# Kernel tuning notes

Hardware: AMD Instinct MI355X
Metric: run time of the kernel (lower is better)

The kernel has to match this reference:

```python
import jax, jax.numpy as jnp
import numpy as np

PATCH = 14
N_HEAD = 8
TOP_K = 2

def _ln(x, g, b, eps=1e-5):
    m = jnp.mean(x, -1, keepdims=True)
    v = jnp.var(x, -1, keepdims=True)
    return (x - m) * jax.lax.rsqrt(v + eps) * g + b

def _mha(x, wq, bq, wk, bk, wv, bv, wo, bo):
    B, S, D = x.shape
    hd = D // N_HEAD
    def split(t):
        return t.reshape(B, S, N_HEAD, hd).transpose(0, 2, 1, 3)
    q = split(x @ wq + bq)
    k = split(x @ wk + bk)
    v = split(x @ wv + bv)
    scores = jnp.einsum('bhqd,bhkd->bhqk', q, k) / jnp.sqrt(jnp.asarray(hd, x.dtype))
    attn = jax.nn.softmax(scores, -1)  # [B,H,S,S]
    out = jnp.einsum('bhqk,bhkd->bhqd', attn, v).transpose(0, 2, 1, 3).reshape(B, S, D)
    return out @ wo + bo, attn

def _moe(x, rw, rb, w1, b1, w2, b2):
    # dense-compute-all-experts-then-mask, matching SparseMoE.forward
    B, S, D = x.shape
    E = rw.shape[1]
    probs = jax.nn.softmax(x @ rw + rb, -1)           # [B,S,E]
    topv, topi = jax.lax.top_k(probs, TOP_K)          # [B,S,K]
    oh = jax.nn.one_hot(topi, E, dtype=x.dtype)       # [B,S,K,E]
    mask = jnp.sum(oh * topv[..., None], -2)          # [B,S,E] top-k gates, zeros elsewhere
    h = jax.nn.gelu(jnp.einsum('bsd,edh->besh', x, w1) + b1[None, :, None, :], approximate=False)
    outs = jnp.einsum('besh,ehd->besd', h, w2) + b2[None, :, None, :]
    out = jnp.einsum('besd,bse->bsd', outs, mask)     # masked sum over experts
    # load-balancing auxiliary loss
    frac = jnp.mean(jnp.sum(oh, -2).reshape(-1, E), 0)
    imp = jnp.mean(probs.reshape(-1, E), 0)
    loss = E * jnp.sum(frac * imp)
    return out, loss

def setup_inputs():
    key = jax.random.key(0)
    B, C, IMG = 32, 3, 224
    D, E, HID = 512, 8, 2048
    S = (IMG // PATCH) ** 2
    PD = C * PATCH * PATCH
    ks = iter(jax.random.split(key, 64))
    def w(shape, fan):
        return jax.random.normal(next(ks), shape, jnp.float32) / np.sqrt(fan).astype(np.float32)
    def moe_params():
        return dict(rw=w((D, E), D), rb=jnp.zeros(E), w1=w((E, D, HID), D), b1=jnp.zeros((E, HID)), w2=w((E, HID, D), HID), b2=jnp.zeros((E, D)))
    m1 = moe_params(); m2 = moe_params()
    return dict(
        x=jax.random.normal(next(ks), (B, C, IMG, IMG), jnp.float32),
        pe_w=w((PD, D), PD), pe_b=jnp.zeros(D),
        pos=w((1, S, D), D),
        ln1_g=jnp.ones(D), ln1_b=jnp.zeros(D),
        ln2_g=jnp.ones(D), ln2_b=jnp.zeros(D),
        ln3_g=jnp.ones(D), ln3_b=jnp.zeros(D),
        wq=w((D, D), D), bq=jnp.zeros(D), wk=w((D, D), D), bk=jnp.zeros(D),
        wv=w((D, D), D), bv=jnp.zeros(D), wo=w((D, D), D), bo=jnp.zeros(D),
        m1_rw=m1['rw'], m1_rb=m1['rb'], m1_w1=m1['w1'], m1_b1=m1['b1'], m1_w2=m1['w2'], m1_b2=m1['b2'],
        m2_rw=m2['rw'], m2_rb=m2['rb'], m2_w1=m2['w1'], m2_b1=m2['b1'], m2_w2=m2['w2'], m2_b2=m2['b2'],
        cls_w=w((D, D), D), cls_b=jnp.zeros(D))

def reference(x, pe_w, pe_b, pos, ln1_g, ln1_b, ln2_g, ln2_b, ln3_g, ln3_b, wq, bq, wk, bk, wv, bv, wo, bo, m1_rw, m1_rb, m1_w1, m1_b1, m1_w2, m1_b2, m2_rw, m2_rb, m2_w1, m2_b1, m2_w2, m2_b2, cls_w, cls_b):
    B, C, H, W = x.shape
    h = H // PATCH
    # einops 'b c (h p1) (w p2) -> b (h w) (p1 p2 c)'
    patches = x.reshape(B, C, h, PATCH, h, PATCH).transpose(0, 2, 4, 3, 5, 1).reshape(B, h * h, PATCH * PATCH * C)
    e = patches @ pe_w + pe_b + pos
    sa, attn = _mha(_ln(e, ln1_g, ln1_b), wq, bq, wk, bk, wv, bv, wo, bo)
    e = e + sa  # dropout is identity at eval
    o1, l1 = _moe(_ln(e, ln2_g, ln2_b), m1_rw, m1_rb, m1_w1, m1_b1, m1_w2, m1_b2)
    o2, l2 = _moe(_ln(o1, ln3_g, ln3_b), m2_rw, m2_rb, m2_w1, m2_b1, m2_w2, m2_b2)
    fv = jnp.mean(o2, 1)
    logits = fv @ cls_w + cls_b
    attn_w = jax.nn.softmax(jnp.mean(attn, 1), -1)  # mean over heads then re-softmax, as in source
    return logits, fv, l1 + l2, attn_w
```

## Files before the change

kernel.cpp:

```cpp
#include <hip/hip_runtime.h>
#include <hip/hip_bf16.h>

using bf16 = __hip_bfloat16;
typedef unsigned short u16;
typedef __attribute__((ext_vector_type(8))) short short8;
typedef __attribute__((ext_vector_type(4))) float f32x4;

#define DEVFN __device__ __forceinline__

DEVFN u16 f2bu(float v) { return __builtin_bit_cast(u16, __float2bfloat16(v)); }
DEVFN float us2f(u16 u) { union { unsigned int i; float f; } x; x.i = ((unsigned int)u) << 16; return x.f; }
DEVFN void unp8(uint4 u, float* f) {
  f[0]=us2f(u.x & 0xffffu); f[1]=us2f(u.x >> 16);
  f[2]=us2f(u.y & 0xffffu); f[3]=us2f(u.y >> 16);
  f[4]=us2f(u.z & 0xffffu); f[5]=us2f(u.z >> 16);
  f[6]=us2f(u.w & 0xffffu); f[7]=us2f(u.w >> 16);
}

DEVFN f32x4 mfma16(short8 a, short8 b, f32x4 c) {
  return __builtin_amdgcn_mfma_f32_16x16x32_bf16(a, b, c, 0, 0, 0);
}

DEVFN void gl16(const u16* g, u16* l) {
  __builtin_amdgcn_global_load_lds((const __attribute__((address_space(1))) void*)g,
                                   (__attribute__((address_space(3))) void*)l, 16, 0, 0);
}

static constexpr size_t OF_PATCH = 0;
static constexpr size_t OF_E     = 4816896;
static constexpr size_t OF_XN    = 9011200;
static constexpr size_t OF_Q     = 13205504;
static constexpr size_t OF_FV    = 38371328;
static constexpr size_t OF_GATES = 38387712;
static constexpr size_t OF_IMPS  = 38404096;
static constexpr size_t OF_CNT   = 38404104;
static constexpr size_t OF_BASE  = 38404112;
static constexpr size_t OF_CURS  = 38404120;
static constexpr size_t OF_LOSS  = 38404128;
static constexpr size_t OF_TOPI  = 38404136;
static constexpr size_t OF_RPOS  = 38420520;
static constexpr size_t OF_RLIST = 38436904;
static constexpr size_t OF_Q16   = 13205504;
static constexpr size_t OF_K16   = 15302656;
static constexpr size_t OF_VT    = 17399808;
static constexpr size_t OF_CTX16 = 19496960;
static constexpr size_t OF_PET   = 21594112;
static constexpr size_t OF_WQT   = 21757952;
static constexpr size_t OF_WKT   = 21889024;
static constexpr size_t OF_WVT   = 22020096;
static constexpr size_t OF_WOT   = 22151168;
static constexpr size_t OF_O1    = 29982720;
static constexpr size_t OF_O2    = 34177024;

__global__ __launch_bounds__(256) void k_patchify(const float* __restrict__ x, u16* __restrict__ XP) {
  int idx = blockIdx.x * 256 + threadIdx.x;
  if (idx >= 8192 * 640) return;
  int row = idx / 640, j = idx - row * 640;
  u16 v = 0;
  if (j < 588) {
    int b = row >> 8, s = row & 255;
    int hh = s >> 4, ww = s & 15;
    int c = j % 3, tt = j / 3;
    int p2 = tt % 14, p1 = tt / 14;
    int src = ((b * 3 + c) * 224 + hh * 14 + p1) * 224 + (ww * 14 + p2);
    v = f2bu(x[src]);
  }
  XP[idx] = v;
}

__global__ __launch_bounds__(256) void k_wcvtd(const float* __restrict__ W, u16* __restrict__ WT, int K, int KP)
{
  __shared__ float s[32][33];
  const int t = threadIdx.x;
  const int tx = t & 31, ty = t >> 5;
  const int k0 = blockIdx.x * 32, n0 = blockIdx.y * 32;
#pragma unroll
  for (int i = 0; i < 4; i++) {
    int kk = k0 + ty + i * 8;
    s[ty + i * 8][tx] = (kk < K) ? W[(size_t)kk * 512 + n0 + tx] : 0.f;
  }
  __syncthreads();
#pragma unroll
  for (int i = 0; i < 4; i++) WT[(size_t)(n0 + ty + i * 8) * KP + k0 + tx] = f2bu(s[tx][ty + i * 8]);
}

__global__ __launch_bounds__(256) void k_wcvt(const float* __restrict__ W, u16* __restrict__ Wt, int K, int N)
{
  __shared__ float s[32][33];
  const int t = threadIdx.x;
  const int tx = t & 31, ty = t >> 5;
  const int k0 = blockIdx.x * 32, n0 = blockIdx.y * 32;
  const size_t es = (size_t)K * N;
  const float* We = W + (size_t)blockIdx.z * es;
  u16* Wte = Wt + (size_t)blockIdx.z * es;
#pragma unroll
  for (int i = 0; i < 4; i++) s[ty + i * 8][tx] = We[(size_t)(k0 + ty + i * 8) * N + n0 + tx];
  __syncthreads();
#pragma unroll
  for (int i = 0; i < 4; i++) Wte[(size_t)(n0 + ty + i * 8) * K + k0 + tx] = f2bu(s[tx][ty + i * 8]);
}

DEVFN void mma_loop(f32x4 acc[4][4], const u16* const agp[4], const u16* const bgp[4],
                    u16* const alp[4], u16* const blp[4], u16* As, u16* Bs,
                    int K, int wm, int wn, int ml, int kq)
{
  for (int k0 = 0; k0 < K; k0 += 64) {
    __syncthreads();
#pragma unroll
    for (int q = 0; q < 4; q++) { gl16(agp[q] + k0, alp[q]); gl16(bgp[q] + k0, blp[q]); }
    __syncthreads();
#pragma unroll
    for (int ks = 0; ks < 2; ks++) {
      const int c = ks * 4 + kq;
      short8 af[4], bf[4];
#pragma unroll
      for (int i = 0; i < 4; i++) {
        const int row = wm + i * 16 + ml;
        af[i] = *(const short8*)&As[row * 64 + ((c ^ (row & 7)) << 3)];
      }
#pragma unroll
      for (int j = 0; j < 4; j++) {
        const int row = wn + j * 16 + ml;
        bf[j] = *(const short8*)&Bs[row * 64 + ((c ^ (row & 7)) << 3)];
      }
#pragma unroll
      for (int i = 0; i < 4; i++)
#pragma unroll
        for (int j = 0; j < 4; j++) acc[i][j] = mfma16(af[i], bf[j], acc[i][j]);
    }
  }
}

DEVFN void ep_xpose(float* ep, const f32x4* ai, int kq, int ml, int er, int ec, float* v)
{
#pragma unroll
  for (int j = 0; j < 4; j++)
#pragma unroll
    for (int r = 0; r < 4; r++)
      ep[(kq * 4 + r) * 68 + j * 16 + ml] = ai[j][r];
  __syncthreads();
#pragma unroll
  for (int u = 0; u < 4; u++) {
    float4 f = *(const float4*)&ep[er * 68 + ec + u * 4];
    v[u * 4 + 0] = f.x; v[u * 4 + 1] = f.y; v[u * 4 + 2] = f.z; v[u * 4 + 3] = f.w;
  }
  __syncthreads();
}

template<int MODE>
__global__ __launch_bounds__(256) void k_bgemm(const u16* __restrict__ A, const u16* __restrict__ BT,
    const float* __restrict__ bias, float* __restrict__ Cf, u16* __restrict__ O16,
    const float* __restrict__ pos, int K)
{
  const int m0 = blockIdx.y * 128, n0 = blockIdx.x * 128;
  __shared__ u16 SB[16384];
  u16* As = SB; u16* Bs = SB + 8192;
  const int t = threadIdx.x;
  const int widx = t >> 6, lane = t & 63;
  const int wm = (widx & 1) * 64, wn = (widx >> 1) * 64;
  const int ml = lane & 15, kq = lane >> 4;
  const u16* agp[4]; const u16* bgp[4]; u16* alp[4]; u16* blp[4];
#pragma unroll
  for (int q = 0; q < 4; q++) {
    const int slot = q * 256 + t;
    const int row = slot >> 3;
    const int c = (slot & 7) ^ (row & 7);
    agp[q] = A + (size_t)(m0 + row) * K + c * 8;
    bgp[q] = BT + (size_t)(n0 + row) * K + c * 8;
    alp[q] = &As[(q * 256 + widx * 64) * 8];
    blp[q] = &Bs[(q * 256 + widx * 64) * 8];
  }
  f32x4 acc[4][4];
#pragma unroll
  for (int i = 0; i < 4; i++)
#pragma unroll
    for (int j = 0; j < 4; j++) acc[i][j] = (f32x4){0.f, 0.f, 0.f, 0.f};
  mma_loop(acc, agp, bgp, alp, blp, As, Bs, K, wm, wn, ml, kq);

  if (MODE == 3) {
#pragma unroll
    for (int j = 0; j < 4; j++) {
      const int n = n0 + wn + j * 16 + ml;
      const float bv = bias[n];
      const int h = n >> 6, d = n & 63;
#pragma unroll
      for (int i = 0; i < 4; i++) {
        const int mb = m0 + wm + i * 16 + kq * 4;
        const int b = mb >> 8, s0 = mb & 255;
        ushort4 w4;
        w4.x = f2bu(acc[i][j][0] + bv); w4.y = f2bu(acc[i][j][1] + bv);
        w4.z = f2bu(acc[i][j][2] + bv); w4.w = f2bu(acc[i][j][3] + bv);
        *(ushort4*)(O16 + ((size_t)(b * 8 + h) * 64 + d) * 256 + s0) = w4;
      }
    }
    return;
  }

  __syncthreads();
  float* ep = (float*)SB + widx * (16 * 68);
  const int er = lane >> 2, ec = (lane & 3) * 16;
  const int gn = n0 + wn + ec;
  float bb[16];
#pragma unroll
  for (int u = 0; u < 4; u++) {
    float4 f = *(const float4*)(bias + gn + u * 4);
    bb[u*4]=f.x; bb[u*4+1]=f.y; bb[u*4+2]=f.z; bb[u*4+3]=f.w;
  }
#pragma unroll
  for (int i = 0; i < 4; i++) {
    float v[16];
    ep_xpose(ep, acc[i], kq, ml, er, ec, v);
    const int gm = m0 + wm + i * 16 + er;
    if (MODE == 0) {
      const float* pr = pos + (size_t)(gm & 255) * 512 + gn;
      float* cp = Cf + (size_t)gm * 512 + gn;
#pragma unroll
      for (int u = 0; u < 4; u++) {
        float4 p = *(const float4*)(pr + u * 4);
        float4 o = {v[u*4]+bb[u*4]+p.x, v[u*4+1]+bb[u*4+1]+p.y, v[u*4+2]+bb[u*4+2]+p.z, v[u*4+3]+bb[u*4+3]+p.w};
        *(float4*)(cp + u * 4) = o;
      }
    } else if (MODE == 1) {
      union { u16 h[16]; uint4 q2[2]; } pk;
#pragma unroll
      for (int u = 0; u < 16; u++) pk.h[u] = f2bu(v[u] + bb[u]);
      u16* hp = O16 + (size_t)gm * 512 + gn;
      *(uint4*)hp = pk.q2[0]; *(uint4*)(hp + 8) = pk.q2[1];
    } else {
      float* cp = Cf + (size_t)gm * 512 + gn;
#pragma unroll
      for (int u = 0; u < 4; u++) {
        float4 oldv = *(const float4*)(cp + u * 4);
        float4 o = {oldv.x+v[u*4]+bb[u*4], oldv.y+v[u*4+1]+bb[u*4+1], oldv.z+v[u*4+2]+bb[u*4+2], oldv.w+v[u*4+3]+bb[u*4+3]};
        *(float4*)(cp + u * 4) = o;
      }
    }
  }
}

__global__ __launch_bounds__(256) void k_ln(const float* __restrict__ X, float* __restrict__ Y,
    u16* __restrict__ YB16, const float* __restrict__ g, const float* __restrict__ b)
{
  __shared__ float red[256];
  const int row = blockIdx.x;
  const int t = threadIdx.x;
  const float* xr = X + (size_t)row * 512;
  float x0 = xr[t], x1 = xr[t + 256];
  red[t] = x0 + x1;
  __syncthreads();
  for (int s = 128; s > 0; s >>= 1) { if (t < s) red[t] += red[t + s]; __syncthreads(); }
  float mean = red[0] * (1.f / 512.f);
  __syncthreads();
  float d0 = x0 - mean, d1 = x1 - mean;
  red[t] = d0 * d0 + d1 * d1;
  __syncthreads();
  for (int s = 128; s > 0; s >>= 1) { if (t < s) red[t] += red[t + s]; __syncthreads(); }
  float rs = 1.f / sqrtf(red[0] * (1.f / 512.f) + 1e-5f);
  float y0 = d0 * rs * g[t]       + b[t];
  float y1 = d1 * rs * g[t + 256] + b[t + 256];
  float* yr = Y + (size_t)row * 512;
  yr[t] = y0; yr[t + 256] = y1;
  u16* br16 = YB16 + (size_t)row * 512;
  br16[t] = f2bu(y0); br16[t + 256] = f2bu(y1);
}

__global__ __launch_bounds__(256) void k_fattn(const u16* __restrict__ Q16, const u16* __restrict__ K16,
    const u16* __restrict__ VT, u16* __restrict__ CTX16, u16* __restrict__ Pg)
{
  __shared__ u16 P[64 * 264];
  __shared__ u16 kv[64 * 136];
  const int t = threadIdx.x;
  const int qt = blockIdx.x, h = blockIdx.y, b = blockIdx.z;
  const int q0 = qt * 64;
  const int lane = t & 63, w = t >> 6;
  const int ml = lane & 15, kq = lane >> 4;
  const int srow = t >> 2, spart = t & 3;

  const size_t tokq = (size_t)(b * 256 + q0 + w * 16 + ml);
  short8 aq0 = *(const short8*)(Q16 + tokq * 512 + h * 64 + kq * 8);
  short8 aq1 = *(const short8*)(Q16 + tokq * 512 + h * 64 + 32 + kq * 8);

  f32x4 sacc[16];
#pragma unroll
  for (int i = 0; i < 16; i++) sacc[i] = (f32x4){0.f, 0.f, 0.f, 0.f};

  for (int kc = 0; kc < 4; kc++) {
    __syncthreads();
    {
      const u16* src = K16 + (size_t)(b * 256 + kc * 64 + srow) * 512 + h * 64 + spart * 16;
      uint4 v0 = *(const uint4*)src;
      uint4 v1 = *(const uint4*)(src + 8);
      *(uint4*)&kv[srow * 72 + spart * 16] = v0;
      *(uint4*)&kv[srow * 72 + spart * 16 + 8] = v1;
    }
    __syncthreads();
#pragma unroll
    for (int kt = 0; kt < 4; kt++) {
      short8 bk0 = *(const short8*)&kv[(kt * 16 + ml) * 72 + kq * 8];
      short8 bk1 = *(const short8*)&kv[(kt * 16 + ml) * 72 + 32 + kq * 8];
      sacc[kc * 4 + kt] = mfma16(aq0, bk0, sacc[kc * 4 + kt]);
      sacc[kc * 4 + kt] = mfma16(aq1, bk1, sacc[kc * 4 + kt]);
    }
  }

#pragma unroll
  for (int r = 0; r < 4; r++) {
    float v[16];
    float mx = -1e30f;
#pragma unroll
    for (int tl = 0; tl < 16; tl++) { v[tl] = sacc[tl][r] * 0.125f; mx = fmaxf(mx, v[tl]); }
#pragma unroll
    for (int mk = 1; mk < 16; mk <<= 1) mx = fmaxf(mx, __shfl_xor(mx, mk, 64));
    float sum = 0.f;
#pragma unroll
    for (int tl = 0; tl < 16; tl++) { v[tl] = __expf(v[tl] - mx); sum += v[tl]; }
#pragma unroll
    for (int mk = 1; mk < 16; mk <<= 1) sum += __shfl_xor(sum, mk, 64);
    float inv = 1.f / sum;
    const int qrow = w * 16 + kq * 4 + r;
#pragma unroll
    for (int tl = 0; tl < 16; tl++) P[qrow * 264 + tl * 16 + ml] = f2bu(v[tl] * inv);
  }
  __syncthreads();

  {
    const int row_l = w * 16 + (lane >> 2);
    const int cp0 = (lane & 3) * 64;
    u16* dst = Pg + ((size_t)(b * 8 + h) * 256 + q0 + row_l) * 256 + cp0;
    const u16* srcl = &P[row_l * 264 + cp0];
#pragma unroll
    for (int i = 0; i < 8; i++) *(uint4*)(dst + i * 8) = *(const uint4*)(srcl + i * 8);
  }

  f32x4 oacc[4];
#pragma unroll
  for (int j = 0; j < 4; j++) oacc[j] = (f32x4){0.f, 0.f, 0.f, 0.f};
  for (int half = 0; half < 2; half++) {
    __syncthreads();
    {
      const u16* src = VT + ((size_t)(b * 8 + h) * 64 + srow) * 256 + half * 128 + spart * 32;
#pragma unroll
      for (int i = 0; i < 4; i++)
        *(uint4*)&kv[srow * 136 + spart * 32 + i * 8] = *(const uint4*)(src + i * 8);
    }
    __syncthreads();
#pragma unroll
    for (int st = 0; st < 4; st++) {
      short8 ap = *(const short8*)&P[(w * 16 + ml) * 264 + half * 128 + st * 32 + kq * 8];
#pragma unroll
      for (int j = 0; j < 4; j++) {
        short8 bv = *(const short8*)&kv[(j * 16 + ml) * 136 + st * 32 + kq * 8];
        oacc[j] = mfma16(ap, bv, oacc[j]);
      }
    }
  }

#pragma unroll
  for (int j = 0; j < 4; j++) {
    const int d = h * 64 + j * 16 + ml;
#pragma unroll
    for (int r = 0; r < 4; r++) {
      const int tok = b * 256 + q0 + w * 16 + kq * 4 + r;
      CTX16[(size_t)tok * 512 + d] = f2bu(oacc[j][r]);
    }
  }
}

__global__ __launch_bounds__(256) void k_attnw(const u16* __restrict__ Pg, float* __restrict__ AW)
{
  const int t = threadIdx.x;
  const int qt = blockIdx.x, b = blockIdx.y;
  const int row = t >> 4, seg = t & 15;
  const int q = qt * 16 + row;
  float vals[16];
#pragma unroll
  for (int i = 0; i < 16; i++) vals[i] = 0.f;
#pragma unroll
  for (int h = 0; h < 8; h++) {
    const u16* src = Pg + ((size_t)(b * 8 + h) * 256 + q) * 256 + seg * 16;
    uint4 u0 = *(const uint4*)src;
    uint4 u1 = *(const uint4*)(src + 8);
    float f0[8], f1[8];
    unp8(u0, f0); unp8(u1, f1);
#pragma unroll
    for (int i = 0; i < 8; i++) { vals[i] += f0[i]; vals[8 + i] += f1[i]; }
  }
  float vmax = -1e30f;
#pragma unroll
  for (int i = 0; i < 16; i++) { vals[i] *= 0.125f; vmax = fmaxf(vmax, vals[i]); }
#pragma unroll
  for (int mk = 1; mk < 16; mk <<= 1) vmax = fmaxf(vmax, __shfl_xor(vmax, mk, 64));
  float ssum = 0.f;
#pragma unroll
  for (int i = 0; i < 16; i++) { vals[i] = __expf(vals[i] - vmax); ssum += vals[i]; }
#pragma unroll
  for (int mk = 1; mk < 16; mk <<= 1) ssum += __shfl_xor(ssum, mk, 64);
  float inv = 1.f / ssum;
  float* orow = AW + (size_t)(b * 256 + q) * 256 + seg * 16;
#pragma unroll
  for (int i = 0; i < 16; i++) orow[i] = vals[i] * inv;
}

DEVFN int rwidx(int k, int e) { return k * 8 + e + (k >> 6) * 4; }

__global__ __launch_bounds__(256) void k_router(const float* __restrict__ XNp, const float* __restrict__ rw,
    const float* __restrict__ rb, float* __restrict__ gates, int* __restrict__ topi,
    int* __restrict__ cnt, float* __restrict__ imps)
{
  __shared__ float rws[4128];
  const int t = threadIdx.x;
  for (int i = t; i < 4096; i += 256) rws[rwidx(i >> 3, i & 7)] = rw[i];
  __syncthreads();
  const int w = t >> 6, l = t & 63;
  const int e = l & 7, ch = l >> 3;
  float impAcc = 0.f; int cntAcc = 0;
  const int row0 = blockIdx.x * 32 + w * 8;
  for (int r = 0; r < 8; r++) {
    const int row = row0 + r;
    const float* xr = XNp + (size_t)row * 512 + ch * 64;
    float s = 0.f;
#pragma unroll 8
    for (int j = 0; j < 64; j++) s = fmaf(xr[j], rws[rwidx(ch * 64 + j, e)], s);
    s += __shfl_xor(s, 8, 64);
    s += __shfl_xor(s, 16, 64);
    s += __shfl_xor(s, 32, 64);
    s += rb[e];
    float p[8];
#pragma unroll
    for (int i = 0; i < 8; i++) p[i] = __shfl(s, (l & 56) | i, 64);
    float mx = p[0];
#pragma unroll
    for (int i = 1; i < 8; i++) mx = fmaxf(mx, p[i]);
    float sum = 0.f;
#pragma unroll
    for (int i = 0; i < 8; i++) { p[i] = __expf(p[i] - mx); sum += p[i]; }
    float inv = 1.f / sum;
#pragma unroll
    for (int i = 0; i < 8; i++) p[i] *= inv;
    int t0 = 0; float v0 = p[0];
#pragma unroll
    for (int i = 1; i < 8; i++) if (p[i] > v0) { v0 = p[i]; t0 = i; }
    int t1 = -1; float v1 = -1.f;
#pragma unroll
    for (int i = 0; i < 8; i++) if (i != t0 && p[i] > v1) { v1 = p[i]; t1 = i; }
    if (l < 8) { impAcc += p[e]; cntAcc += (t0 == e) + (t1 == e); }
    if (l == 0) {
      gates[(size_t)row * 2] = v0; gates[(size_t)row * 2 + 1] = v1;
      topi[(size_t)row * 2] = t0;  topi[(size_t)row * 2 + 1] = t1;
    }
  }
  if (l < 8) { atomicAdd(&imps[e], impAcc); atomicAdd(&cnt[e], cntAcc); }
}

__global__ void k_scan(const int* __restrict__ cnt, int* __restrict__ basep, int* __restrict__ curs) {
  if (threadIdx.x == 0) {
    int a = 0;
    for (int e = 0; e < 8; e++) { basep[e] = a; a += cnt[e]; }
  }
  if (threadIdx.x < 8) curs[threadIdx.x] = 0;
}

__global__ __launch_bounds__(256) void k_scatter(const int* __restrict__ topi, const int* __restrict__ basep,
    int* __restrict__ cursor, int* __restrict__ rowlist, int* __restrict__ rowpos)
{
  __shared__ int lcnt[8], lbase[8];
  const int t = threadIdx.x;
  if (t < 8) lcnt[t] = 0;
  __syncthreads();
  const int token = blockIdx.x * 256 + t;
  const int e0 = topi[token * 2], e1 = topi[token * 2 + 1];
  const int p0 = atomicAdd(&lcnt[e0], 1);
  const int p1 = atomicAdd(&lcnt[e1], 1);
  __syncthreads();
  if (t < 8) lbase[t] = atomicAdd(&cursor[t], lcnt[t]);
  __syncthreads();
  const int pos0 = basep[e0] + lbase[e0] + p0;
  const int pos1 = basep[e1] + lbase[e1] + p1;
  rowlist[pos0] = token; rowlist[pos1] = token;
  rowpos[token * 2] = pos0; rowpos[token * 2 + 1] = pos1;
}

__global__ void k_loss(const int* __restrict__ cnt, const float* __restrict__ imps,
                       float* __restrict__ lossws, float* __restrict__ out, int phase) {
  if (threadIdx.x == 0 && blockIdx.x == 0) {
    float s = 0.f;
    for (int e = 0; e < 8; e++) s += ((float)cnt[e]) * imps[e];
    s *= 8.f / (8192.f * 8192.f);
    if (phase == 0) *lossws = s;
    else out[0] = *lossws + s;
  }
}

__global__ __launch_bounds__(256) void k_mg1(const u16* __restrict__ XNB, const u16* __restrict__ W1T,
    const float* __restrict__ B1, u16* __restrict__ H,
    const int* __restrict__ rowlist, const int* __restrict__ basep, const int* __restrict__ cntp)
{
  const int e = blockIdx.z;
  const int cnt = cntp[e];
  const int m0 = blockIdx.y * 128;
  if (m0 >= cnt) return;
  const int base = basep[e];
  const int n0 = blockIdx.x * 128;
  __shared__ u16 SB[16384];
  __shared__ int rl[128];
  u16* As = SB; u16* Bs = SB + 8192;
  const int t = threadIdx.x;
  if (t < 128) rl[t] = rowlist[base + min(m0 + t, cnt - 1)];
  __syncthreads();
  const int widx = t >> 6, lane = t & 63;
  const int wm = (widx & 1) * 64, wn = (widx >> 1) * 64;
  const int ml = lane & 15, kq = lane >> 4;
  const u16* wt = W1T + (size_t)e * (2048 * 512);
  const u16* agp[4]; const u16* bgp[4]; u16* alp[4]; u16* blp[4];
#pragma unroll
  for (int q = 0; q < 4; q++) {
    const int slot = q * 256 + t;
    const int row = slot >> 3;
    const int c = (slot & 7) ^ (row & 7);
    agp[q] = XNB + (size_t)rl[row] * 512 + c * 8;
    bgp[q] = wt + (size_t)(n0 + row) * 512 + c * 8;
    alp[q] = &As[(q * 256 + widx * 64) * 8];
    blp[q] = &Bs[(q * 256 + widx * 64) * 8];
  }
  f32x4 acc[4][4];
#pragma unroll
  for (int i = 0; i < 4; i++)
#pragma unroll
    for (int j = 0; j < 4; j++) acc[i][j] = (f32x4){0.f, 0.f, 0.f, 0.f};
  mma_loop(acc, agp, bgp, alp, blp, As, Bs, 512, wm, wn, ml, kq);

  __syncthreads();
  float* ep = (float*)SB + widx * (16 * 68);
  const int er = lane >> 2, ec = (lane & 3) * 16;
  const int gn = n0 + wn + ec;
  float bb[16];
#pragma unroll
  for (int u = 0; u < 4; u++) {
    float4 f = *(const float4*)(B1 + e * 2048 + gn + u * 4);
    bb[u*4]=f.x; bb[u*4+1]=f.y; bb[u*4+2]=f.z; bb[u*4+3]=f.w;
  }
#pragma unroll
  for (int i = 0; i < 4; i++) {
    float v[16];
    ep_xpose(ep, acc[i], kq, ml, er, ec, v);
    const int lr = wm + i * 16 + er;
    if (m0 + lr < cnt) {
      union { u16 h[16]; uint4 q2[2]; } pk;
#pragma unroll
      for (int u = 0; u < 16; u++) {
        float vv = v[u] + bb[u];
        float g = 0.5f * vv * (1.f + erff(vv * 0.70710678118654752f));
        pk.h[u] = f2bu(g);
      }
      u16* hp = H + (size_t)(base + m0 + lr) * 2048 + gn;
      *(uint4*)hp = pk.q2[0]; *(uint4*)(hp + 8) = pk.q2[1];
    }
  }
}

__global__ __launch_bounds__(256) void k_mg2(const u16* __restrict__ H, const u16* __restrict__ W2T,
    const float* __restrict__ B2, float* __restrict__ YB,
    const int* __restrict__ basep, const int* __restrict__ cntp)
{
  const int e = blockIdx.z;
  const int cnt = cntp[e];
  const int m0 = blockIdx.y * 128;
  if (m0 >= cnt) return;
  const int base = basep[e];
  const int n0 = blockIdx.x * 128;
  __shared__ u16 SB[16384];
  u16* As = SB; u16* Bs = SB + 8192;
  const int t = threadIdx.x;
  const int widx = t >> 6, lane = t & 63;
  const int wm = (widx & 1) * 64, wn = (widx >> 1) * 64;
  const int ml = lane & 15, kq = lane >> 4;
  const u16* wt = W2T + (size_t)e * (512 * 2048);
  const u16* agp[4]; const u16* bgp[4]; u16* alp[4]; u16* blp[4];
#pragma unroll
  for (int q = 0; q < 4; q++) {
    const int slot = q * 256 + t;
    const int row = slot >> 3;
    const int c = (slot & 7) ^ (row & 7);
    const int gr = min(base + m0 + row, 16383);
    agp[q] = H + (size_t)gr * 2048 + c * 8;
    bgp[q] = wt + (size_t)(n0 + row) * 2048 + c * 8;
    alp[q] = &As[(q * 256 + widx * 64) * 8];
    blp[q] = &Bs[(q * 256 + widx * 64) * 8];
  }
  f32x4 acc[4][4];
#pragma unroll
  for (int i = 0; i < 4; i++)
#pragma unroll
    for (int j = 0; j < 4; j++) acc[i][j] = (f32x4){0.f, 0.f, 0.f, 0.f};
  mma_loop(acc, agp, bgp, alp, blp, As, Bs, 2048, wm, wn, ml, kq);

  __syncthreads();
  float* ep = (float*)SB + widx * (16 * 68);
  const int er = lane >> 2, ec = (lane & 3) * 16;
  const int gn = n0 + wn + ec;
  float bb[16];
#pragma unroll
  for (int u = 0; u < 4; u++) {
    float4 f = *(const float4*)(B2 + e * 512 + gn + u * 4);
    bb[u*4]=f.x; bb[u*4+1]=f.y; bb[u*4+2]=f.z; bb[u*4+3]=f.w;
  }
#pragma unroll
  for (int i = 0; i < 4; i++) {
    float v[16];
    ep_xpose(ep, acc[i], kq, ml, er, ec, v);
    const int lr = wm + i * 16 + er;
    if (m0 + lr < cnt) {
      float* yp = YB + (size_t)(base + m0 + lr) * 512 + gn;
#pragma unroll
      for (int u = 0; u < 4; u++) {
        float4 o = {v[u*4]+bb[u*4], v[u*4+1]+bb[u*4+1], v[u*4+2]+bb[u*4+2], v[u*4+3]+bb[u*4+3]};
        *(float4*)(yp + u * 4) = o;
      }
    }
  }
}

__global__ __launch_bounds__(256) void k_combine(const float* __restrict__ YB, const float* __restrict__ gates,
    const int* __restrict__ rowpos, float* __restrict__ OUT)
{
  const int idx = blockIdx.x * 256 + threadIdx.x;
  const int row = idx >> 9, d = idx & 511;
  const float g0 = gates[row * 2], g1 = gates[row * 2 + 1];
  const int r0 = rowpos[row * 2], r1 = rowpos[row * 2 + 1];
  OUT[idx] = g0 * YB[(size_t)r0 * 512 + d] + g1 * YB[(size_t)r1 * 512 + d];
}

__global__ __launch_bounds__(256) void k_fv(const float* __restrict__ O2, float* __restrict__ FVp, float* __restrict__ outv) {
  const int idx = blockIdx.x * 256 + threadIdx.x;
  const int b = idx >> 9, d = idx & 511;
  const float* p = O2 + (size_t)b * 131072 + d;
  float s = 0.f;
  for (int i = 0; i < 256; i++) s += p[i * 512];
  s *= (1.f / 256.f);
  FVp[idx] = s;
  outv[idx] = s;
}

__global__ __launch_bounds__(256) void k_cls(const float* __restrict__ FVp, const float* __restrict__ W,
    const float* __restrict__ bias, float* __restrict__ outl) {
  const int idx = blockIdx.x * 256 + threadIdx.x;
  const int b = idx >> 9, n = idx & 511;
  const float* f = FVp + (size_t)b * 512;
  float s = 0.f;
  for (int d = 0; d < 512; d++) s = fmaf(f[d], W[(size_t)d * 512 + n], s);
  s += bias[n];
  outl[idx] = s;
}

extern "C" void kernel_launch(void* const* d_in, const int* in_sizes, int n_in,
                              void* d_out, int out_size, void* d_ws, size_t ws_size,
                              hipStream_t stream)
{
  (void)in_sizes; (void)n_in; (void)out_size; (void)ws_size;
  const float* x    = (const float*)d_in[0];
  const float* pe_w = (const float*)d_in[1];
  const float* pe_b = (const float*)d_in[2];
  const float* pos  = (const float*)d_in[3];
  const float* ln1g = (const float*)d_in[4];
  const float* ln1b = (const float*)d_in[5];
  const float* lng[2] = {(const float*)d_in[6], (const float*)d_in[8]};
  const float* lnb[2] = {(const float*)d_in[7], (const float*)d_in[9]};
  const float* wq = (const float*)d_in[10]; const float* bq = (const float*)d_in[11];
  const float* wk = (const float*)d_in[12]; const float* bk = (const float*)d_in[13];
  const float* wv = (const float*)d_in[14]; const float* bv = (const float*)d_in[15];
  const float* wo = (const float*)d_in[16]; const float* bo = (const float*)d_in[17];
  const float* m_rw[2] = {(const float*)d_in[18], (const float*)d_in[24]};
  const float* m_rb[2] = {(const float*)d_in[19], (const float*)d_in[25]};
  const float* m_w1[2] = {(const float*)d_in[20], (const float*)d_in[26]};
  const float* m_b1[2] = {(const float*)d_in[21], (const float*)d_in[27]};
  const float* m_w2[2] = {(const float*)d_in[22], (const float*)d_in[28]};
  const float* m_b2[2] = {(const float*)d_in[23], (const float*)d_in[29]};
  const float* cls_w = (const float*)d_in[30];
  const float* cls_b = (const float*)d_in[31];

  float* ws = (float*)d_ws;
  u16* XP    = (u16*)(ws + OF_PATCH);
  float* ebuf = ws + OF_E;
  float* xn   = ws + OF_XN;
  u16* Q16   = (u16*)(ws + OF_Q16);
  u16* K16   = (u16*)(ws + OF_K16);
  u16* VTb   = (u16*)(ws + OF_VT);
  u16* ctx16 = (u16*)(ws + OF_CTX16);
  u16* peT   = (u16*)(ws + OF_PET);
  u16* wqT   = (u16*)(ws + OF_WQT);
  u16* wkT   = (u16*)(ws + OF_WKT);
  u16* wvT   = (u16*)(ws + OF_WVT);
  u16* woT   = (u16*)(ws + OF_WOT);
  u16* Pgb   = (u16*)(ws + OF_O1);
  float* o1   = ws + OF_O1;
  float* o2   = ws + OF_O2;
  float* fv   = ws + OF_FV;
  float* gates = ws + OF_GATES;
  float* imps  = ws + OF_IMPS;
  int* cnt    = (int*)(ws + OF_CNT);
  int* basep  = (int*)(ws + OF_BASE);
  int* curs   = (int*)(ws + OF_CURS);
  float* lossws = ws + OF_LOSS;
  int* topi   = (int*)(ws + OF_TOPI);
  int* rowpos = (int*)(ws + OF_RPOS);
  int* rowlist= (int*)(ws + OF_RLIST);
  u16* Hbuf  = (u16*)(ws + OF_Q);
  float* YB  = ws + OF_PATCH;
  u16* XNB   = (u16*)(ws + OF_PATCH);
  u16* W1T   = (u16*)(ws + OF_O1);
  u16* W2T   = (u16*)(ws + OF_O2);

  float* out = (float*)d_out;
  float* out_logits = out;
  float* out_fv     = out + 16384;
  float* out_loss   = out + 32768;
  float* out_attnw  = out + 32769;

  k_wcvtd<<<dim3(20, 16), 256, 0, stream>>>(pe_w, peT, 588, 640);
  k_wcvtd<<<dim3(16, 16), 256, 0, stream>>>(wq, wqT, 512, 512);
  k_wcvtd<<<dim3(16, 16), 256, 0, stream>>>(wk, wkT, 512, 512);
  k_wcvtd<<<dim3(16, 16), 256, 0, stream>>>(wv, wvT, 512, 512);
  k_wcvtd<<<dim3(16, 16), 256, 0, stream>>>(wo, woT, 512, 512);

  k_patchify<<<20480, 256, 0, stream>>>(x, XP);
  k_bgemm<0><<<dim3(4, 64), 256, 0, stream>>>(XP, peT, pe_b, ebuf, nullptr, pos, 640);
  k_ln<<<8192, 256, 0, stream>>>(ebuf, xn, XNB, ln1g, ln1b);
  k_bgemm<1><<<dim3(4, 64), 256, 0, stream>>>(XNB, wqT, bq, nullptr, Q16, nullptr, 512);
  k_bgemm<1><<<dim3(4, 64), 256, 0, stream>>>(XNB, wkT, bk, nullptr, K16, nullptr, 512);
  k_bgemm<3><<<dim3(4, 64), 256, 0, stream>>>(XNB, wvT, bv, nullptr, VTb, nullptr, 512);
  k_fattn<<<dim3(4, 8, 32), 256, 0, stream>>>(Q16, K16, VTb, ctx16, Pgb);
  k_attnw<<<dim3(16, 32), 256, 0, stream>>>(Pgb, out_attnw);
  k_bgemm<2><<<dim3(4, 64), 256, 0, stream>>>(ctx16, woT, bo, ebuf, nullptr, nullptr, 512);

  const float* moe_in[2] = {ebuf, o1};
  float* moe_out[2] = {o1, o2};
  for (int mi = 0; mi < 2; mi++) {
    hipMemsetAsync(imps, 0, 64, stream);
    k_ln<<<8192, 256, 0, stream>>>(moe_in[mi], xn, XNB, lng[mi], lnb[mi]);
    k_wcvt<<<dim3(16, 64, 8), 256, 0, stream>>>(m_w1[mi], W1T, 512, 2048);
    k_wcvt<<<dim3(64, 16, 8), 256, 0, stream>>>(m_w2[mi], W2T, 2048, 512);
    k_router<<<256, 256, 0, stream>>>(xn, m_rw[mi], m_rb[mi], gates, topi, cnt, imps);
    k_scan<<<1, 64, 0, stream>>>(cnt, basep, curs);
    k_scatter<<<32, 256, 0, stream>>>(topi, basep, curs, rowlist, rowpos);
    k_loss<<<1, 64, 0, stream>>>(cnt, imps, lossws, out_loss, mi);
    k_mg1<<<dim3(16, 64, 8), 256, 0, stream>>>(XNB, W1T, m_b1[mi], Hbuf, rowlist, basep, cnt);
    k_mg2<<<dim3(4, 64, 8), 256, 0, stream>>>(Hbuf, W2T, m_b2[mi], YB, basep, cnt);
    k_combine<<<16384, 256, 0, stream>>>(YB, gates, rowpos, moe_out[mi]);
  }
  k_fv<<<64, 256, 0, stream>>>(o2, fv, out_fv);
  k_cls<<<64, 256, 0, stream>>>(fv, cls_w, cls_b, out_logits);
}
```

Before: 942.7 us.

## Double-buffer LDS tiles in GEMM main loop to overlap loads with MFMA

Restructures the shared GEMM k-loop into a ping-pong scheme with two LDS buffers. The next tile's global-to-LDS loads are issued before computing on the current tile, which removes one barrier per iteration and hides load latency. LDS use per block doubles to 64KB, which may lower occupancy on the dense and MoE expert GEMM kernels. The loop assumes an even number of 64-wide k tiles.

```diff
diff --git a/kernel.cpp b/kernel.cpp
--- a/kernel.cpp
+++ b/kernel.cpp
@@ -100,35 +100,62 @@
   for (int i = 0; i < 4; i++) Wte[(size_t)(n0 + ty + i * 8) * K + k0 + tx] = f2bu(s[tx][ty + i * 8]);
 }
 
+DEVFN void mma_stage(const u16* const agp[4], const u16* const bgp[4],
+                     u16* Asb, u16* Bsb, int k0, int widx)
+{
+#pragma unroll
+  for (int q = 0; q < 4; q++) {
+    gl16(agp[q] + k0, Asb + (q * 256 + widx * 64) * 8);
+    gl16(bgp[q] + k0, Bsb + (q * 256 + widx * 64) * 8);
+  }
+}
+
+DEVFN void mma_step(f32x4 acc[4][4], const u16* As, const u16* Bs,
+                    int wm, int wn, int ml, int kq)
+{
+#pragma unroll
+  for (int ks = 0; ks < 2; ks++) {
+    const int c = ks * 4 + kq;
+    short8 af[4], bf[4];
+#pragma unroll
+    for (int i = 0; i < 4; i++) {
+      const int row = wm + i * 16 + ml;
+      af[i] = *(const short8*)&As[row * 64 + ((c ^ (row & 7)) << 3)];
+    }
+#pragma unroll
+    for (int j = 0; j < 4; j++) {
+      const int row = wn + j * 16 + ml;
+      bf[j] = *(const short8*)&Bs[row * 64 + ((c ^ (row & 7)) << 3)];
+    }
+#pragma unroll
+    for (int i = 0; i < 4; i++)
+#pragma unroll
+      for (int j = 0; j < 4; j++) acc[i][j] = mfma16(af[i], bf[j], acc[i][j]);
+  }
+}
+
 DEVFN void mma_loop(f32x4 acc[4][4], const u16* const agp[4], const u16* const bgp[4],
-                    u16* const alp[4], u16* const blp[4], u16* As, u16* Bs,
-                    int K, int wm, int wn, int ml, int kq)
-{
-  for (int k0 = 0; k0 < K; k0 += 64) {
+                    u16* SB, int K, int wm, int wn, int ml, int kq, int widx)
+{
+  u16* As0 = SB;          u16* Bs0 = SB + 8192;
+  u16* As1 = SB + 16384;  u16* Bs1 = SB + 24576;
+  const int NT = K >> 6;
+  mma_stage(agp, bgp, As0, Bs0, 0, widx);
+  __syncthreads();
+  int k = 64;
+  for (int t = 0; t + 2 < NT; t += 2) {
+    mma_stage(agp, bgp, As1, Bs1, k, widx);
+    mma_step(acc, As0, Bs0, wm, wn, ml, kq);
     __syncthreads();
-#pragma unroll
-    for (int q = 0; q < 4; q++) { gl16(agp[q] + k0, alp[q]); gl16(bgp[q] + k0, blp[q]); }
+    mma_stage(agp, bgp, As0, Bs0, k + 64, widx);
+    mma_step(acc, As1, Bs1, wm, wn, ml, kq);
     __syncthreads();
-#pragma unroll
-    for (int ks = 0; ks < 2; ks++) {
-      const int c = ks * 4 + kq;
-      short8 af[4], bf[4];
-#pragma unroll
-      for (int i = 0; i < 4; i++) {
-        const int row = wm + i * 16 + ml;
-        af[i] = *(const short8*)&As[row * 64 + ((c ^ (row & 7)) << 3)];
-      }
-#pragma unroll
-      for (int j = 0; j < 4; j++) {
-        const int row = wn + j * 16 + ml;
-        bf[j] = *(const short8*)&Bs[row * 64 + ((c ^ (row & 7)) << 3)];
-      }
-#pragma unroll
-      for (int i = 0; i < 4; i++)
-#pragma unroll
-        for (int j = 0; j < 4; j++) acc[i][j] = mfma16(af[i], bf[j], acc[i][j]);
-    }
-  }
+    k += 128;
+  }
+  mma_stage(agp, bgp, As1, Bs1, k, widx);
+  mma_step(acc, As0, Bs0, wm, wn, ml, kq);
+  __syncthreads();
+  mma_step(acc, As1, Bs1, wm, wn, ml, kq);
 }
 
 DEVFN void ep_xpose(float* ep, const f32x4* ai, int kq, int ml, int er, int ec, float* v)
@@ -153,13 +180,12 @@
     const float* __restrict__ pos, int K)
 {
   const int m0 = blockIdx.y * 128, n0 = blockIdx.x * 128;
-  __shared__ u16 SB[16384];
-  u16* As = SB; u16* Bs = SB + 8192;
+  __shared__ alignas(16) u16 SB[32768];
   const int t = threadIdx.x;
   const int widx = t >> 6, lane = t & 63;
   const int wm = (widx & 1) * 64, wn = (widx >> 1) * 64;
   const int ml = lane & 15, kq = lane >> 4;
-  const u16* agp[4]; const u16* bgp[4]; u16* alp[4]; u16* blp[4];
+  const u16* agp[4]; const u16* bgp[4];
 #pragma unroll
   for (int q = 0; q < 4; q++) {
     const int slot = q * 256 + t;
@@ -167,15 +193,13 @@
     const int c = (slot & 7) ^ (row & 7);
     agp[q] = A + (size_t)(m0 + row) * K + c * 8;
     bgp[q] = BT + (size_t)(n0 + row) * K + c * 8;
-    alp[q] = &As[(q * 256 + widx * 64) * 8];
-    blp[q] = &Bs[(q * 256 + widx * 64) * 8];
   }
   f32x4 acc[4][4];
 #pragma unroll
   for (int i = 0; i < 4; i++)
 #pragma unroll
     for (int j = 0; j < 4; j++) acc[i][j] = (f32x4){0.f, 0.f, 0.f, 0.f};
-  mma_loop(acc, agp, bgp, alp, blp, As, Bs, K, wm, wn, ml, kq);
+  mma_loop(acc, agp, bgp, SB, K, wm, wn, ml, kq, widx);
 
   if (MODE == 3) {
 #pragma unroll
@@ -501,9 +525,8 @@
   if (m0 >= cnt) return;
   const int base = basep[e];
   const int n0 = blockIdx.x * 128;
-  __shared__ u16 SB[16384];
+  __shared__ alignas(16) u16 SB[32768];
   __shared__ int rl[128];
-  u16* As = SB; u16* Bs = SB + 8192;
   const int t = threadIdx.x;
   if (t < 128) rl[t] = rowlist[base + min(m0 + t, cnt - 1)];
   __syncthreads();
@@ -511,7 +534,7 @@
   const int wm = (widx & 1) * 64, wn = (widx >> 1) * 64;
   const int ml = lane & 15, kq = lane >> 4;
   const u16* wt = W1T + (size_t)e * (2048 * 512);
-  const u16* agp[4]; const u16* bgp[4]; u16* alp[4]; u16* blp[4];
+  const u16* agp[4]; const u16* bgp[4];
 #pragma unroll
   for (int q = 0; q < 4; q++) {
     const int slot = q * 256 + t;
@@ -519,15 +542,13 @@
     const int c = (slot & 7) ^ (row & 7);
     agp[q] = XNB + (size_t)rl[row] * 512 + c * 8;
     bgp[q] = wt + (size_t)(n0 + row) * 512 + c * 8;
-    alp[q] = &As[(q * 256 + widx * 64) * 8];
-    blp[q] = &Bs[(q * 256 + widx * 64) * 8];
   }
   f32x4 acc[4][4];
 #pragma unroll
   for (int i = 0; i < 4; i++)
 #pragma unroll
     for (int j = 0; j < 4; j++) acc[i][j] = (f32x4){0.f, 0.f, 0.f, 0.f};
-  mma_loop(acc, agp, bgp, alp, blp, As, Bs, 512, wm, wn, ml, kq);
+  mma_loop(acc, agp, bgp, SB, 512, wm, wn, ml, kq, widx);
 
   __syncthreads();
   float* ep = (float*)SB + widx * (16 * 68);
@@ -568,14 +589,13 @@
   if (m0 >= cnt) return;
   const int base = basep[e];
   const int n0 = blockIdx.x * 128;
-  __shared__ u16 SB[16384];
-  u16* As = SB; u16* Bs = SB + 8192;
+  __shared__ alignas(16) u16 SB[32768];
   const int t = threadIdx.x;
   const int widx = t >> 6, lane = t & 63;
   const int wm = (widx & 1) * 64, wn = (widx >> 1) * 64;
   const int ml = lane & 15, kq = lane >> 4;
   const u16* wt = W2T + (size_t)e * (512 * 2048);
-  const u16* agp[4]; const u16* bgp[4]; u16* alp[4]; u16* blp[4];
+  const u16* agp[4]; const u16* bgp[4];
 #pragma unroll
   for (int q = 0; q < 4; q++) {
     const int slot = q * 256 + t;
@@ -584,15 +604,13 @@
     const int gr = min(base + m0 + row, 16383);
     agp[q] = H + (size_t)gr * 2048 + c * 8;
     bgp[q] = wt + (size_t)(n0 + row) * 2048 + c * 8;
-    alp[q] = &As[(q * 256 + widx * 64) * 8];
-    blp[q] = &Bs[(q * 256 + widx * 64) * 8];
   }
   f32x4 acc[4][4];
 #pragma unroll
   for (int i = 0; i < 4; i++)
 #pragma unroll
     for (int j = 0; j < 4; j++) acc[i][j] = (f32x4){0.f, 0.f, 0.f, 0.f};
-  mma_loop(acc, agp, bgp, alp, blp, As, Bs, 2048, wm, wn, ml, kq);
+  mma_loop(acc, agp, bgp, SB, 2048, wm, wn, ml, kq, widx);
 
   __syncthreads();
   float* ep = (float*)SB + widx * (16 * 68);
```

Result: faster. 871.2 us (-7.6%).
